# Kernel tuning notes

Hardware: AMD Instinct MI355X
Metric: run time of the kernel (lower is better)

Reference implementation:

```python
import jax, jax.numpy as jnp
import numpy as np

EPS = 1e-5  # BatchNorm eps


def _mlp(x, w1, b1, w2, b2, g, bt):
    # NRI MLP: elu(fc1) -> elu(fc2) -> batchnorm over all leading dims (training-mode batch stats)
    h = jax.nn.elu(x @ w1.T + b1)
    h = jax.nn.elu(h @ w2.T + b2)
    f = h.reshape(-1, h.shape[-1])
    mu = f.mean(0)
    var = f.var(0)  # biased, as in torch BN normalization
    return (h - mu) * jax.lax.rsqrt(var + EPS) * g + bt


def _gru(x, w_ih, w_hh, b_ih, b_hh):
    # x: [B, T, D] batch_first; torch GRU gate order (r, z, n)
    gi = jnp.einsum('btd,hd->bth', x, w_ih) + b_ih  # precompute input gates
    H = w_hh.shape[1]
    h0 = jnp.zeros((x.shape[0], H), x.dtype)

    def step(h, gi_t):
        gh = h @ w_hh.T + b_hh
        ir, iz, inn = jnp.split(gi_t, 3, -1)
        hr, hz, hn = jnp.split(gh, 3, -1)
        r = jax.nn.sigmoid(ir + hr)
        z = jax.nn.sigmoid(iz + hz)
        n = jnp.tanh(inn + r * hn)
        h_new = (1.0 - z) * n + z * h
        return h_new, h_new

    hT, ys = jax.lax.scan(step, h0, gi.transpose(1, 0, 2))
    return ys.transpose(1, 0, 2), hT


def _xavier(key, shape):
    std = np.sqrt(2.0 / (shape[0] + shape[1])).astype(np.float32)
    return jax.random.normal(key, shape, jnp.float32) * std


def setup_inputs() -> dict:
    key = jax.random.key(0)
    ks = iter(jax.random.split(key, 64))
    B, N, T, Fin, H, O = 8, 30, 100, 4, 128, 2
    inputs = jax.random.normal(next(ks), (B, N, T, Fin), jnp.float32)
    r, s = np.nonzero(1 - np.eye(N))  # fully connected, no self loops -> E = N*(N-1)
    eye = np.eye(N, dtype=np.float32)
    d = {
        'inputs': inputs,
        'rel_rec': jnp.asarray(eye[r]),
        'rel_send': jnp.asarray(eye[s]),
    }
    dims = {1: Fin, 2: 2 * H, 3: H, 4: 3 * H}
    for k in (1, 2, 3, 4):
        d[f'm{k}_w1'] = _xavier(next(ks), (H, dims[k]))
        d[f'm{k}_b1'] = jnp.full((H,), 0.1, jnp.float32)
        d[f'm{k}_w2'] = _xavier(next(ks), (H, H))
        d[f'm{k}_b2'] = jnp.full((H,), 0.1, jnp.float32)
        d[f'm{k}_g'] = jnp.ones((H,), jnp.float32)
        d[f'm{k}_bt'] = jnp.zeros((H,), jnp.float32)
    u = float(1.0 / np.sqrt(H))
    for p in ('gf', 'gr'):
        d[f'{p}_wih'] = jax.random.uniform(next(ks), (3 * H, H), jnp.float32, -u, u)
        d[f'{p}_whh'] = jax.random.uniform(next(ks), (3 * H, H), jnp.float32, -u, u)
        d[f'{p}_bih'] = jax.random.uniform(next(ks), (3 * H,), jnp.float32, -u, u)
        d[f'{p}_bhh'] = jax.random.uniform(next(ks), (3 * H,), jnp.float32, -u, u)
    d['pw'] = _xavier(next(ks), (O, H))
    d['pb'] = jnp.full((O,), 0.1, jnp.float32)
    d['ew'] = _xavier(next(ks), (O, 2 * H))
    d['eb'] = jnp.full((O,), 0.1, jnp.float32)
    return d


def reference(inputs, rel_rec, rel_send, m1_w1, m1_b1, m1_w2, m1_b2, m1_g, m1_bt, m2_w1, m2_b1, m2_w2, m2_b2, m2_g, m2_bt, m3_w1, m3_b1, m3_w2, m3_b2, m3_g, m3_bt, m4_w1, m4_b1, m4_w2, m4_b2, m4_g, m4_bt, gf_wih, gf_whh, gf_bih, gf_bhh, gr_wih, gr_whh, gr_bih, gr_bhh, pw, pb, ew, eb):
    N = rel_rec.shape[1]

    def node2edge(x):  # x: [B,N,T,H] -> [B,E,T,2H]
        snd = jnp.einsum('en,bnth->beth', rel_send, x)
        rcv = jnp.einsum('en,bnth->beth', rel_rec, x)
        return jnp.concatenate([snd, rcv], -1)

    def edge2node(x):  # x: [B,E,T,H] -> [B,N,T,H], mean-style normalization by N
        return jnp.einsum('en,beth->bnth', rel_rec, x) / N

    x = _mlp(inputs, m1_w1, m1_b1, m1_w2, m1_b2, m1_g, m1_bt)      # [B,N,T,H]
    x = node2edge(x)                                                # [B,E,T,2H]
    x = _mlp(x, m2_w1, m2_b1, m2_w2, m2_b2, m2_g, m2_bt)            # [B,E,T,H]
    x_skip = x
    x = edge2node(x)                                                # [B,N,T,H]
    x = _mlp(x, m3_w1, m3_b1, m3_w2, m3_b2, m3_g, m3_bt)
    x = node2edge(x)                                                # [B,E,T,2H]
    x = jnp.concatenate([x, x_skip], -1)                            # [B,E,T,3H]
    x = _mlp(x, m4_w1, m4_b1, m4_w2, m4_b2, m4_g, m4_bt)            # [B,E,T,H]

    B, E, T, H = x.shape
    xr = x.reshape(B * E, T, H)
    fwd_x, hT = _gru(xr, gf_wih, gf_whh, gf_bih, gf_bhh)
    rev_x, _ = _gru(xr[:, ::-1], gr_wih, gr_whh, gr_bih, gr_bhh)
    rev_x = rev_x[:, ::-1]

    prior = (fwd_x @ pw.T + pb).reshape(B, E, T, -1)
    comb = jnp.concatenate([fwd_x, rev_x], -1)
    enc = (comb @ ew.T + eb).reshape(B, E, T, -1)
    return prior, enc, hT[None]  # hT[None] matches torch GRU h_n [1, B*E, H]
```

## Files before the change

kernel.cpp:

```cpp
#include <hip/hip_runtime.h>
#include <math.h>

typedef float f32x4 __attribute__((ext_vector_type(4)));
typedef short bf16x8 __attribute__((ext_vector_type(8)));
typedef unsigned int uint32;
#define DEV static __device__ __forceinline__

constexpr int B_ = 8, N_ = 30, T_ = 100, FIN = 4, H_ = 128;
constexpr int E_ = N_*(N_-1);
constexpr int NSEQ = B_*E_;
constexpr int RN = B_*N_*T_;
constexpr int RE = B_*E_*T_;
constexpr int ET = E_*T_;
constexpr int NB_GRU = (NSEQ + 63)/64;

DEV float eluf(float x){ return x > 0.f ? x : __expf(x) - 1.f; }
DEV float sigmoidf(float x){ return 1.f/(1.f + __expf(-x)); }
DEV float tanhfast(float x){
  float cx = fminf(fmaxf(x, -20.f), 20.f);
  float e = __expf(2.f*cx);
  return (e - 1.f)/(e + 1.f);
}
DEV float dot4(f32x4 a, f32x4 b){ return a[0]*b[0] + a[1]*b[1] + a[2]*b[2] + a[3]*b[3]; }

DEV float bf2f(unsigned short u){ return __uint_as_float(((uint32)u) << 16); }
DEV uint32 f2bf_bits(float f){ uint32 b = __float_as_uint(f); return (b + 0x7FFFu + ((b >> 16) & 1u)) >> 16; }
DEV uint32 pack2(float lo, float hi){ return f2bf_bits(lo) | (f2bf_bits(hi) << 16); }

DEV bf16x8 cvt8(const float* __restrict__ p){
  f32x4 a = *(const f32x4*)p;
  f32x4 b = *(const f32x4*)(p+4);
  bf16x8 r;
  r[0]=(short)f2bf_bits(a[0]); r[1]=(short)f2bf_bits(a[1]);
  r[2]=(short)f2bf_bits(a[2]); r[3]=(short)f2bf_bits(a[3]);
  r[4]=(short)f2bf_bits(b[0]); r[5]=(short)f2bf_bits(b[1]);
  r[6]=(short)f2bf_bits(b[2]); r[7]=(short)f2bf_bits(b[3]);
  return r;
}

DEV void edge_decomp(int row, int& b, int& t, int& sn, int& ir)
{
  b = row / ET;
  int rem = row - b*ET;
  int e   = rem / T_;
  t = rem - e*T_;
  ir = e / (N_-1);
  int j = e - ir*(N_-1);
  sn = j + (j >= ir ? 1 : 0);
}

DEV int xcd_swizzle(int orig, int nwg)
{
  int q = nwg >> 3, r = nwg & 7;
  int xcd = orig & 7, j = orig >> 3;
  return (xcd < r ? xcd*(q+1) : r*(q+1) + (xcd-r)*q) + j;
}

__global__ __launch_bounds__(256)
void prep_weights(const float* __restrict__ w21, const float* __restrict__ w22,
                  const float* __restrict__ w41, const float* __restrict__ w42,
                  unsigned short* __restrict__ wbf)
{
  int idx = blockIdx.x*256 + threadIdx.x;
  if (idx >= 114688) return;
  float v;
  if (idx < 32768)      v = w21[idx];
  else if (idx < 49152) v = w22[idx - 32768];
  else if (idx < 98304) v = w41[idx - 49152];
  else                  v = w42[idx - 98304];
  wbf[idx] = (unsigned short)f2bf_bits(v);
}

template<int MODE, int DIN>
__global__ __launch_bounds__(256)
void mlp_fused(const float* __restrict__ src,
               const float* __restrict__ w1, const float* __restrict__ b1,
               const float* __restrict__ w2, const float* __restrict__ b2,
               float* __restrict__ out)
{
  constexpr int KC  = (DIN < 32) ? DIN : 32;
  constexpr int NCH = DIN / KC;
  __shared__ float As[KC][68];
  __shared__ float Ws[32][132];
  __shared__ float Hs[128][68];

  const int tid  = threadIdx.x;
  const int row0 = blockIdx.x * 64;
  const int tx = tid & 15, ty = tid >> 4;
  const int c0 = tx*8, r0 = ty*4;

  float acc[4][8];
  #pragma unroll
  for (int j=0;j<4;++j){
    #pragma unroll
    for (int i=0;i<8;++i) acc[j][i]=0.f;
  }

  for (int ch = 0; ch < NCH; ++ch) {
    for (int idx = tid; idx < 64*KC; idx += 256) {
      int r = idx / KC, k = idx % KC;
      As[k][r] = src[(size_t)(row0 + r)*DIN + ch*KC + k];
    }
    for (int idx = tid; idx < 128*KC; idx += 256) {
      int o = idx / KC, k = idx % KC;
      Ws[k][o] = w1[o*DIN + ch*KC + k];
    }
    __syncthreads();
    #pragma unroll
    for (int k = 0; k < KC; ++k) {
      f32x4 a  = *(const f32x4*)&As[k][r0];
      f32x4 wA = *(const f32x4*)&Ws[k][c0];
      f32x4 wB = *(const f32x4*)&Ws[k][c0+4];
      #pragma unroll
      for (int j=0;j<4;++j){
        #pragma unroll
        for (int i=0;i<4;++i){
          acc[j][i]   += a[j]*wA[i];
          acc[j][4+i] += a[j]*wB[i];
        }
      }
    }
    __syncthreads();
  }
  {
    #pragma unroll
    for (int i=0;i<8;++i){
      float bb = b1[c0+i];
      #pragma unroll
      for (int j=0;j<4;++j)
        Hs[c0+i][r0+j] = eluf(acc[j][i] + bb);
    }
  }
  __syncthreads();

  #pragma unroll
  for (int j=0;j<4;++j){
    #pragma unroll
    for (int i=0;i<8;++i) acc[j][i]=0.f;
  }

  for (int ch = 0; ch < 4; ++ch) {
    for (int idx = tid; idx < 128*32; idx += 256) {
      int o = idx >> 5, k = idx & 31;
      Ws[k][o] = w2[o*H_ + ch*32 + k];
    }
    __syncthreads();
    #pragma unroll
    for (int k = 0; k < 32; ++k) {
      f32x4 a  = *(const f32x4*)&Hs[ch*32 + k][r0];
      f32x4 wA = *(const f32x4*)&Ws[k][c0];
      f32x4 wB = *(const f32x4*)&Ws[k][c0+4];
      #pragma unroll
      for (int j=0;j<4;++j){
        #pragma unroll
        for (int i=0;i<4;++i){
          acc[j][i]   += a[j]*wA[i];
          acc[j][4+i] += a[j]*wB[i];
        }
      }
    }
    __syncthreads();
  }
  {
    #pragma unroll
    for (int j=0;j<4;++j){
      size_t base = (size_t)(row0 + r0 + j)*H_ + c0;
      #pragma unroll
      for (int i=0;i<8;++i) out[base+i] = eluf(acc[j][i] + b2[c0+i]);
    }
  }
}

__global__ __launch_bounds__(128)
void norm_to_bf16(const float* __restrict__ buf, int rows, const float* __restrict__ sums,
                  const float* __restrict__ g, const float* __restrict__ bt,
                  unsigned short* __restrict__ outbf)
{
  int c = threadIdx.x;
  float inv = 1.f/(float)rows;
  float mu  = sums[c]*inv;
  float var = sums[H_+c]*inv - mu*mu;
  float sc  = rsqrtf(var + 1e-5f)*g[c];
  float sh  = bt[c] - mu*sc;
  for (int r = blockIdx.x; r < rows; r += gridDim.x) {
    size_t idx = (size_t)r*H_ + c;
    outbf[idx] = (unsigned short)f2bf_bits(buf[idx]*sc + sh);
  }
}

__global__ __launch_bounds__(256)
void apply_aff4(unsigned short* __restrict__ x4, const float* __restrict__ aff)
{
  size_t idx = ((size_t)blockIdx.x*256 + threadIdx.x)*8;
  int c = (int)(idx & 127);
  uint32* p = (uint32*)(x4 + idx);
  uint32 win[4];
  #pragma unroll
  for (int u=0;u<4;++u) win[u] = p[u];
  uint32 o[4];
  #pragma unroll
  for (int u=0;u<4;++u){
    float lo = __uint_as_float(win[u] << 16);
    float hi = __uint_as_float(win[u] & 0xFFFF0000u);
    float a = lo*aff[c+2*u]   + aff[128+c+2*u];
    float b = hi*aff[c+2*u+1] + aff[128+c+2*u+1];
    o[u] = pack2(a, b);
  }
  #pragma unroll
  for (int u=0;u<4;++u) p[u] = o[u];
}

__global__ __launch_bounds__(256, 2)
void mlp2_scatter(const unsigned short* __restrict__ x1bf,
                  const unsigned short* __restrict__ wbf,
                  const float* __restrict__ b21, const float* __restrict__ b22,
                  float* __restrict__ nodeB, float* __restrict__ stats2)
{
  __shared__ int srow[64], rrow[64];
  __shared__ __align__(16) char pool[17408];
  unsigned short* bufH = (unsigned short*)pool;
  float* red = (float*)pool;

  const int tid  = threadIdx.x;
  const int bid  = xcd_swizzle(blockIdx.x, gridDim.x);
  const int row0 = bid * 64;
  if (tid < 64) {
    int b,t,sn,ir; edge_decomp(row0 + tid, b, t, sn, ir);
    srow[tid] = (b*N_ + sn)*T_ + t;
    rrow[tid] = (b*N_ + ir)*T_ + t;
  }
  __syncthreads();

  const int lane = tid & 63;
  const int wv   = tid >> 6;
  const int c15  = lane & 15;
  const int k8   = (lane >> 4) * 8;
  const int g4   = (lane >> 4);
  const int colb = wv * 32;
  const unsigned short* W21 = wbf;
  const unsigned short* W22 = wbf + 32768;

  int sA[4], rA[4];
  #pragma unroll
  for (int rt=0;rt<4;++rt){ sA[rt] = srow[rt*16 + c15]; rA[rt] = rrow[rt*16 + c15]; }

  f32x4 C[2][4];

  #pragma unroll
  for (int ci=0;ci<2;++ci){
    float bb = b21[colb + ci*16 + c15];
    #pragma unroll
    for (int rt=0;rt<4;++rt) C[ci][rt] = (f32x4){bb,bb,bb,bb};
  }
  {
    bf16x8 Bf[2][8];
    #pragma unroll
    for (int ci=0;ci<2;++ci){
      #pragma unroll
      for (int kc=0;kc<8;++kc)
        Bf[ci][kc] = *(const bf16x8*)&W21[(size_t)(colb+ci*16+c15)*256 + kc*32 + k8];
    }
    #pragma unroll
    for (int kc=0;kc<8;++kc){
      bf16x8 A[4];
      #pragma unroll
      for (int rt=0;rt<4;++rt){
        int nrow = (kc<4) ? sA[rt] : rA[rt];
        A[rt] = *(const bf16x8*)&x1bf[(size_t)nrow*H_ + (kc&3)*32 + k8];
      }
      #pragma unroll
      for (int ci=0;ci<2;++ci){
        #pragma unroll
        for (int rt=0;rt<4;++rt)
          C[ci][rt] = __builtin_amdgcn_mfma_f32_16x16x32_bf16(A[rt], Bf[ci][kc], C[ci][rt], 0,0,0);
      }
    }
  }
  #pragma unroll
  for (int ci=0;ci<2;++ci){
    #pragma unroll
    for (int rt=0;rt<4;++rt){
      #pragma unroll
      for (int rr=0;rr<4;++rr){
        int row = rt*16 + g4*4 + rr;
        bufH[row*136 + colb + ci*16 + c15] = (unsigned short)f2bf_bits(eluf(C[ci][rt][rr]));
      }
    }
  }
  __syncthreads();

  #pragma unroll
  for (int ci=0;ci<2;++ci){
    float bb = b22[colb + ci*16 + c15];
    #pragma unroll
    for (int rt=0;rt<4;++rt) C[ci][rt] = (f32x4){bb,bb,bb,bb};
  }
  {
    bf16x8 Bf[2][4];
    #pragma unroll
    for (int ci=0;ci<2;++ci){
      #pragma unroll
      for (int kc=0;kc<4;++kc)
        Bf[ci][kc] = *(const bf16x8*)&W22[(size_t)(colb+ci*16+c15)*128 + kc*32 + k8];
    }
    #pragma unroll
    for (int kc=0;kc<4;++kc){
      bf16x8 A[4];
      #pragma unroll
      for (int rt=0;rt<4;++rt)
        A[rt] = *(const bf16x8*)&bufH[(rt*16+c15)*136 + kc*32 + k8];
      #pragma unroll
      for (int ci=0;ci<2;++ci){
        #pragma unroll
        for (int rt=0;rt<4;++rt)
          C[ci][rt] = __builtin_amdgcn_mfma_f32_16x16x32_bf16(A[rt], Bf[ci][kc], C[ci][rt], 0,0,0);
      }
    }
  }

  float s1l[2], s2l[2];
  #pragma unroll
  for (int ci=0;ci<2;++ci){ s1l[ci]=0.f; s2l[ci]=0.f; }
  #pragma unroll
  for (int ci=0;ci<2;++ci){
    int col = colb + ci*16 + c15;
    #pragma unroll
    for (int rt=0;rt<4;++rt){
      #pragma unroll
      for (int rr=0;rr<4;++rr){
        int row = rt*16 + g4*4 + rr;
        float v = eluf(C[ci][rt][rr]);
        atomicAdd(&nodeB[(size_t)rrow[row]*H_ + col], v);
        s1l[ci] += v; s2l[ci] += v*v;
      }
    }
  }
  __syncthreads();
  #pragma unroll
  for (int ci=0;ci<2;++ci){
    int col = colb + ci*16 + c15;
    red[col*4 + g4]       = s1l[ci];
    red[512 + col*4 + g4] = s2l[ci];
  }
  __syncthreads();
  if (tid < 128) {
    float s=0.f, q=0.f;
    #pragma unroll
    for (int u=0;u<4;++u){ s += red[tid*4+u]; q += red[512 + tid*4+u]; }
    atomicAdd(&stats2[tid], s);
    atomicAdd(&stats2[128+tid], q);
  }
}

__global__ __launch_bounds__(256, 2)
void mlp24_fused(const unsigned short* __restrict__ x1bf, const unsigned short* __restrict__ x3bf,
                 const float* __restrict__ aff2, const unsigned short* __restrict__ wbf,
                 const float* __restrict__ b21, const float* __restrict__ b22,
                 const float* __restrict__ b41, const float* __restrict__ b42,
                 unsigned short* __restrict__ x4pre, float* __restrict__ stats4)
{
  __shared__ int srow[64], rrow[64];
  __shared__ __align__(16) char pool[34816];
  unsigned short* bufH = (unsigned short*)pool;
  unsigned short* bufX = (unsigned short*)(pool + 17408);
  float* red = (float*)pool;

  const int tid  = threadIdx.x;
  const int bid  = xcd_swizzle(blockIdx.x, gridDim.x);
  const int row0 = bid * 64;
  if (tid < 64) {
    int b,t,sn,ir; edge_decomp(row0 + tid, b, t, sn, ir);
    srow[tid] = (b*N_ + sn)*T_ + t;
    rrow[tid] = (b*N_ + ir)*T_ + t;
  }
  __syncthreads();

  const int lane = tid & 63;
  const int wv   = tid >> 6;
  const int c15  = lane & 15;
  const int k8   = (lane >> 4) * 8;
  const int g4   = (lane >> 4);
  const int colb = wv * 32;
  const unsigned short* W21 = wbf;
  const unsigned short* W22 = wbf + 32768;
  const unsigned short* W41 = wbf + 49152;
  const unsigned short* W42 = wbf + 98304;

  int sA[4], rA[4];
  #pragma unroll
  for (int rt=0;rt<4;++rt){ sA[rt] = srow[rt*16 + c15]; rA[rt] = rrow[rt*16 + c15]; }

  f32x4 C[2][4];

  #pragma unroll
  for (int ci=0;ci<2;++ci){
    float bb = b21[colb + ci*16 + c15];
    #pragma unroll
    for (int rt=0;rt<4;++rt) C[ci][rt] = (f32x4){bb,bb,bb,bb};
  }
  {
    bf16x8 Bf[2][8];
    #pragma unroll
    for (int ci=0;ci<2;++ci){
      #pragma unroll
      for (int kc=0;kc<8;++kc)
        Bf[ci][kc] = *(const bf16x8*)&W21[(size_t)(colb+ci*16+c15)*256 + kc*32 + k8];
    }
    #pragma unroll
    for (int kc=0;kc<8;++kc){
      bf16x8 A[4];
      #pragma unroll
      for (int rt=0;rt<4;++rt){
        int nrow = (kc<4) ? sA[rt] : rA[rt];
        A[rt] = *(const bf16x8*)&x1bf[(size_t)nrow*H_ + (kc&3)*32 + k8];
      }
      #pragma unroll
      for (int ci=0;ci<2;++ci){
        #pragma unroll
        for (int rt=0;rt<4;++rt)
          C[ci][rt] = __builtin_amdgcn_mfma_f32_16x16x32_bf16(A[rt], Bf[ci][kc], C[ci][rt], 0,0,0);
      }
    }
  }
  #pragma unroll
  for (int ci=0;ci<2;++ci){
    #pragma unroll
    for (int rt=0;rt<4;++rt){
      #pragma unroll
      for (int rr=0;rr<4;++rr){
        int row = rt*16 + g4*4 + rr;
        bufH[row*136 + colb + ci*16 + c15] = (unsigned short)f2bf_bits(eluf(C[ci][rt][rr]));
      }
    }
  }
  __syncthreads();

  #pragma unroll
  for (int ci=0;ci<2;++ci){
    float bb = b22[colb + ci*16 + c15];
    #pragma unroll
    for (int rt=0;rt<4;++rt) C[ci][rt] = (f32x4){bb,bb,bb,bb};
  }
  {
    bf16x8 Bf[2][4];
    #pragma unroll
    for (int ci=0;ci<2;++ci){
      #pragma unroll
      for (int kc=0;kc<4;++kc)
        Bf[ci][kc] = *(const bf16x8*)&W22[(size_t)(colb+ci*16+c15)*128 + kc*32 + k8];
    }
    #pragma unroll
    for (int kc=0;kc<4;++kc){
      bf16x8 A[4];
      #pragma unroll
      for (int rt=0;rt<4;++rt)
        A[rt] = *(const bf16x8*)&bufH[(rt*16+c15)*136 + kc*32 + k8];
      #pragma unroll
      for (int ci=0;ci<2;++ci){
        #pragma unroll
        for (int rt=0;rt<4;++rt)
          C[ci][rt] = __builtin_amdgcn_mfma_f32_16x16x32_bf16(A[rt], Bf[ci][kc], C[ci][rt], 0,0,0);
      }
    }
  }
  #pragma unroll
  for (int ci=0;ci<2;++ci){
    int col = colb + ci*16 + c15;
    float sc = aff2[col], sh = aff2[128+col];
    #pragma unroll
    for (int rt=0;rt<4;++rt){
      #pragma unroll
      for (int rr=0;rr<4;++rr){
        int row = rt*16 + g4*4 + rr;
        bufX[row*136 + col] = (unsigned short)f2bf_bits(eluf(C[ci][rt][rr])*sc + sh);
      }
    }
  }
  __syncthreads();

  #pragma unroll
  for (int ci=0;ci<2;++ci){
    float bb = b41[colb + ci*16 + c15];
    #pragma unroll
    for (int rt=0;rt<4;++rt) C[ci][rt] = (f32x4){bb,bb,bb,bb};
  }
  {
    bf16x8 Bf[2][6];
    #pragma unroll
    for (int ci=0;ci<2;++ci){
      #pragma unroll
      for (int kc=0;kc<6;++kc)
        Bf[ci][kc] = *(const bf16x8*)&W41[(size_t)(colb+ci*16+c15)*384 + kc*32 + k8];
    }
    #pragma unroll
    for (int kc=0;kc<6;++kc){
      bf16x8 A[4];
      #pragma unroll
      for (int rt=0;rt<4;++rt){
        if (kc < 4) A[rt] = *(const bf16x8*)&x3bf[(size_t)sA[rt]*H_ + kc*32 + k8];
        else        A[rt] = *(const bf16x8*)&x3bf[(size_t)rA[rt]*H_ + (kc-4)*32 + k8];
      }
      #pragma unroll
      for (int ci=0;ci<2;++ci){
        #pragma unroll
        for (int rt=0;rt<4;++rt)
          C[ci][rt] = __builtin_amdgcn_mfma_f32_16x16x32_bf16(A[rt], Bf[ci][kc], C[ci][rt], 0,0,0);
      }
    }
    #pragma unroll
    for (int ci=0;ci<2;++ci){
      #pragma unroll
      for (int kc=0;kc<6;++kc)
        Bf[ci][kc] = *(const bf16x8*)&W41[(size_t)(colb+ci*16+c15)*384 + (kc+6)*32 + k8];
    }
    #pragma unroll
    for (int kc=6;kc<12;++kc){
      bf16x8 A[4];
      #pragma unroll
      for (int rt=0;rt<4;++rt){
        if (kc < 8) A[rt] = *(const bf16x8*)&x3bf[(size_t)rA[rt]*H_ + (kc-4)*32 + k8];
        else        A[rt] = *(const bf16x8*)&bufX[(rt*16+c15)*136 + (kc-8)*32 + k8];
      }
      #pragma unroll
      for (int ci=0;ci<2;++ci){
        #pragma unroll
        for (int rt=0;rt<4;++rt)
          C[ci][rt] = __builtin_amdgcn_mfma_f32_16x16x32_bf16(A[rt], Bf[ci][kc-6], C[ci][rt], 0,0,0);
      }
    }
  }
  __syncthreads();
  #pragma unroll
  for (int ci=0;ci<2;++ci){
    #pragma unroll
    for (int rt=0;rt<4;++rt){
      #pragma unroll
      for (int rr=0;rr<4;++rr){
        int row = rt*16 + g4*4 + rr;
        bufH[row*136 + colb + ci*16 + c15] = (unsigned short)f2bf_bits(eluf(C[ci][rt][rr]));
      }
    }
  }
  __syncthreads();

  #pragma unroll
  for (int ci=0;ci<2;++ci){
    float bb = b42[colb + ci*16 + c15];
    #pragma unroll
    for (int rt=0;rt<4;++rt) C[ci][rt] = (f32x4){bb,bb,bb,bb};
  }
  {
    bf16x8 Bf[2][4];
    #pragma unroll
    for (int ci=0;ci<2;++ci){
      #pragma unroll
      for (int kc=0;kc<4;++kc)
        Bf[ci][kc] = *(const bf16x8*)&W42[(size_t)(colb+ci*16+c15)*128 + kc*32 + k8];
    }
    #pragma unroll
    for (int kc=0;kc<4;++kc){
      bf16x8 A[4];
      #pragma unroll
      for (int rt=0;rt<4;++rt)
        A[rt] = *(const bf16x8*)&bufH[(rt*16+c15)*136 + kc*32 + k8];
      #pragma unroll
      for (int ci=0;ci<2;++ci){
        #pragma unroll
        for (int rt=0;rt<4;++rt)
          C[ci][rt] = __builtin_amdgcn_mfma_f32_16x16x32_bf16(A[rt], Bf[ci][kc], C[ci][rt], 0,0,0);
      }
    }
  }
  float s1l[2], s2l[2];
  #pragma unroll
  for (int ci=0;ci<2;++ci){ s1l[ci]=0.f; s2l[ci]=0.f; }
  #pragma unroll
  for (int ci=0;ci<2;++ci){
    int col = colb + ci*16 + c15;
    #pragma unroll
    for (int rt=0;rt<4;++rt){
      #pragma unroll
      for (int rr=0;rr<4;++rr){
        int row = rt*16 + g4*4 + rr;
        float v = eluf(C[ci][rt][rr]);
        x4pre[(size_t)(row0 + row)*H_ + col] = (unsigned short)f2bf_bits(v);
        s1l[ci] += v; s2l[ci] += v*v;
      }
    }
  }
  __syncthreads();
  #pragma unroll
  for (int ci=0;ci<2;++ci){
    int col = colb + ci*16 + c15;
    red[col*4 + g4]       = s1l[ci];
    red[512 + col*4 + g4] = s2l[ci];
  }
  __syncthreads();
  if (tid < 128) {
    float s=0.f, q=0.f;
    #pragma unroll
    for (int u=0;u<4;++u){ s += red[tid*4+u]; q += red[512 + tid*4+u]; }
    atomicAdd(&stats4[tid], s);
    atomicAdd(&stats4[128+tid], q);
  }
}

__global__ __launch_bounds__(128)
void stats_kernel(const float* __restrict__ buf, int rows, float* __restrict__ sums)
{
  int c = threadIdx.x;
  float s = 0.f, s2 = 0.f;
  for (int r = blockIdx.x; r < rows; r += gridDim.x) {
    float v = buf[(size_t)r*H_ + c];
    s += v; s2 += v*v;
  }
  atomicAdd(&sums[c], s);
  atomicAdd(&sums[H_ + c], s2);
}

__global__ __launch_bounds__(128)
void finalize_aff(const float* __restrict__ sums, const float* __restrict__ g,
                  const float* __restrict__ bt, float* __restrict__ aff, int rows)
{
  int c = threadIdx.x;
  float inv = 1.f/(float)rows;
  float mu  = sums[c]*inv;
  float var = sums[H_+c]*inv - mu*mu;
  float sc  = rsqrtf(var + 1e-5f)*g[c];
  aff[c]      = sc;
  aff[H_ + c] = bt[c] - mu*sc;
}

__global__ __launch_bounds__(256)
void e2n_finalize(float* __restrict__ nodeB, const float* __restrict__ aff2)
{
  int idx = blockIdx.x*256 + threadIdx.x;
  if (idx >= RN*H_) return;
  int c = idx & 127;
  nodeB[idx] = (nodeB[idx]*aff2[c] + (float)(N_-1)*aff2[128+c]) * (1.f/(float)N_);
}

__global__ __launch_bounds__(512, 1)
void gru_kernel(const unsigned short* __restrict__ x4n,
                const float* __restrict__ wihf, const float* __restrict__ whhf,
                const float* __restrict__ bihf, const float* __restrict__ bhhf,
                const float* __restrict__ wihr, const float* __restrict__ whhr,
                const float* __restrict__ bihr, const float* __restrict__ bhhr,
                const float* __restrict__ pw, const float* __restrict__ pb,
                const float* __restrict__ ew, const float* __restrict__ eb,
                float* __restrict__ out_prior, float* __restrict__ out_enc,
                float* __restrict__ out_hT)
{
  __shared__ __align__(16) unsigned short As[64*264];
  __shared__ __align__(16) float hs[64*132];
  __shared__ float pws[256];
  __shared__ float ews[512];

  const int tid  = threadIdx.x;
  const int dir  = blockIdx.x / NB_GRU;
  const int blk  = blockIdx.x % NB_GRU;
  const int seq0 = blk * 64;
  const int lane = tid & 63;
  const int wv   = __builtin_amdgcn_readfirstlane(tid >> 6);
  const int j0   = wv * 16;
  const int c15  = lane & 15;
  const int k8g  = (lane >> 4) * 8;

  const float* wih = dir ? wihr : wihf;
  const float* whh = dir ? whhr : whhf;
  const float* bih = dir ? bihr : bihf;
  const float* bhh = dir ? bhhr : bhhf;

  bf16x8 Br[8], Bz[8], Bi[4], Bn[4];
  #pragma unroll
  for (int kt=0; kt<8; ++kt){
    const float* sr = (kt<4) ? (wih + (size_t)(j0+c15)*H_ + kt*32 + k8g)
                             : (whh + (size_t)(j0+c15)*H_ + (kt-4)*32 + k8g);
    Br[kt] = cvt8(sr);
    const float* sz = (kt<4) ? (wih + (size_t)(128+j0+c15)*H_ + kt*32 + k8g)
                             : (whh + (size_t)(128+j0+c15)*H_ + (kt-4)*32 + k8g);
    Bz[kt] = cvt8(sz);
  }
  #pragma unroll
  for (int kt=0; kt<4; ++kt){
    Bi[kt] = cvt8(wih + (size_t)(256+j0+c15)*H_ + kt*32 + k8g);
    Bn[kt] = cvt8(whh + (size_t)(256+j0+c15)*H_ + kt*32 + k8g);
  }
  const float bR = bih[j0+c15]     + bhh[j0+c15];
  const float bZ = bih[128+j0+c15] + bhh[128+j0+c15];
  const float bI = bih[256+j0+c15];
  const float bN = bhh[256+j0+c15];
  const float pb0 = pb[0], pb1 = pb[1], eb0 = eb[0], eb1 = eb[1];

  for (int i = tid; i < 64*264; i += 512) As[i] = 0;
  for (int i = tid; i < 64*132; i += 512) hs[i] = 0.f;
  for (int i = tid; i < 256; i += 512) pws[i] = pw[i];
  for (int i = tid; i < 512; i += 512) ews[i] = ew[i];
  float hreg[16];
  #pragma unroll
  for (int i=0;i<16;++i) hreg[i] = 0.f;

  const int ss = tid >> 3;
  const int cc = (tid & 7) * 16;
  const int qq = seq0 + ss;

  uint32 xw[8];
  {
    int t0 = dir ? (T_-1) : 0;
    if (qq < NSEQ) {
      const uint32* gp = (const uint32*)(x4n + ((size_t)qq*T_ + t0)*H_ + cc);
      #pragma unroll
      for (int u=0;u<8;++u) xw[u] = gp[u];
    } else {
      #pragma unroll
      for (int u=0;u<8;++u) xw[u] = 0;
    }
  }
  __syncthreads();

  for (int step = 0; step < T_; ++step) {
    const int t = dir ? (T_-1-step) : step;

    {
      uint32* xp = (uint32*)(As + ss*264 + cc);
      #pragma unroll
      for (int u=0;u<8;++u) xp[u] = xw[u];
    }
    __syncthreads();

    if (step + 1 < T_) {
      int tn = dir ? (T_-2-step) : (step+1);
      if (qq < NSEQ) {
        const uint32* gp = (const uint32*)(x4n + ((size_t)qq*T_ + tn)*H_ + cc);
        #pragma unroll
        for (int u=0;u<8;++u) xw[u] = gp[u];
      }
    }

    f32x4 Cr[4], Cz[4], Ci[4], Cn[4];
    #pragma unroll
    for (int rt=0;rt<4;++rt){
      Cr[rt] = (f32x4){bR,bR,bR,bR};
      Cz[rt] = (f32x4){bZ,bZ,bZ,bZ};
      Ci[rt] = (f32x4){bI,bI,bI,bI};
      Cn[rt] = (f32x4){bN,bN,bN,bN};
    }
    #pragma unroll
    for (int kt=0; kt<8; ++kt){
      bf16x8 a0 = *(const bf16x8*)&As[(size_t)( 0+c15)*264 + kt*32 + k8g];
      bf16x8 a1 = *(const bf16x8*)&As[(size_t)(16+c15)*264 + kt*32 + k8g];
      bf16x8 a2 = *(const bf16x8*)&As[(size_t)(32+c15)*264 + kt*32 + k8g];
      bf16x8 a3 = *(const bf16x8*)&As[(size_t)(48+c15)*264 + kt*32 + k8g];
      Cr[0] = __builtin_amdgcn_mfma_f32_16x16x32_bf16(a0, Br[kt], Cr[0], 0,0,0);
      Cr[1] = __builtin_amdgcn_mfma_f32_16x16x32_bf16(a1, Br[kt], Cr[1], 0,0,0);
      Cr[2] = __builtin_amdgcn_mfma_f32_16x16x32_bf16(a2, Br[kt], Cr[2], 0,0,0);
      Cr[3] = __builtin_amdgcn_mfma_f32_16x16x32_bf16(a3, Br[kt], Cr[3], 0,0,0);
      Cz[0] = __builtin_amdgcn_mfma_f32_16x16x32_bf16(a0, Bz[kt], Cz[0], 0,0,0);
      Cz[1] = __builtin_amdgcn_mfma_f32_16x16x32_bf16(a1, Bz[kt], Cz[1], 0,0,0);
      Cz[2] = __builtin_amdgcn_mfma_f32_16x16x32_bf16(a2, Bz[kt], Cz[2], 0,0,0);
      Cz[3] = __builtin_amdgcn_mfma_f32_16x16x32_bf16(a3, Bz[kt], Cz[3], 0,0,0);
      if (kt < 4) {
        Ci[0] = __builtin_amdgcn_mfma_f32_16x16x32_bf16(a0, Bi[kt], Ci[0], 0,0,0);
        Ci[1] = __builtin_amdgcn_mfma_f32_16x16x32_bf16(a1, Bi[kt], Ci[1], 0,0,0);
        Ci[2] = __builtin_amdgcn_mfma_f32_16x16x32_bf16(a2, Bi[kt], Ci[2], 0,0,0);
        Ci[3] = __builtin_amdgcn_mfma_f32_16x16x32_bf16(a3, Bi[kt], Ci[3], 0,0,0);
      } else {
        Cn[0] = __builtin_amdgcn_mfma_f32_16x16x32_bf16(a0, Bn[kt-4], Cn[0], 0,0,0);
        Cn[1] = __builtin_amdgcn_mfma_f32_16x16x32_bf16(a1, Bn[kt-4], Cn[1], 0,0,0);
        Cn[2] = __builtin_amdgcn_mfma_f32_16x16x32_bf16(a2, Bn[kt-4], Cn[2], 0,0,0);
        Cn[3] = __builtin_amdgcn_mfma_f32_16x16x32_bf16(a3, Bn[kt-4], Cn[3], 0,0,0);
      }
    }
    __syncthreads();

    #pragma unroll
    for (int rt=0;rt<4;++rt){
      #pragma unroll
      for (int rr=0;rr<4;++rr){
        float r_ = sigmoidf(Cr[rt][rr]);
        float z_ = sigmoidf(Cz[rt][rr]);
        float n_ = tanhfast(Ci[rt][rr] + r_*Cn[rt][rr]);
        float hn = (1.f - z_)*n_ + z_*hreg[rt*4+rr];
        hreg[rt*4+rr] = hn;
        int row = rt*16 + (lane>>4)*4 + rr;
        As[(size_t)row*264 + 128 + j0 + c15] = (unsigned short)f2bf_bits(hn);
        hs[row*132 + j0 + c15] = hn;
      }
    }
    __syncthreads();

    if (qq < NSEQ) {
      const f32x4* hrow = (const f32x4*)(hs + ss*132 + cc);
      f32x4 h0=hrow[0], h1=hrow[1], h2=hrow[2], h3=hrow[3];
      size_t obase = ((size_t)qq*T_ + t)*2;
      if (dir == 0) {
        const f32x4* pw0 = (const f32x4*)(pws + cc);
        const f32x4* pw1 = (const f32x4*)(pws + H_ + cc);
        const f32x4* ew0 = (const f32x4*)(ews + cc);
        const f32x4* ew1 = (const f32x4*)(ews + 2*H_ + cc);
        float p0 = dot4(pw0[0],h0)+dot4(pw0[1],h1)+dot4(pw0[2],h2)+dot4(pw0[3],h3);
        float p1 = dot4(pw1[0],h0)+dot4(pw1[1],h1)+dot4(pw1[2],h2)+dot4(pw1[3],h3);
        float e0 = dot4(ew0[0],h0)+dot4(ew0[1],h1)+dot4(ew0[2],h2)+dot4(ew0[3],h3);
        float e1 = dot4(ew1[0],h0)+dot4(ew1[1],h1)+dot4(ew1[2],h2)+dot4(ew1[3],h3);
        #pragma unroll
        for (int m=1;m<8;m<<=1){
          p0 += __shfl_xor(p0,m); p1 += __shfl_xor(p1,m);
          e0 += __shfl_xor(e0,m); e1 += __shfl_xor(e1,m);
        }
        if ((tid & 7) == 0) {
          out_prior[obase]   = p0 + pb0;
          out_prior[obase+1] = p1 + pb1;
          atomicAdd(&out_enc[obase],   e0);
          atomicAdd(&out_enc[obase+1], e1);
        }
      } else {
        const f32x4* ew0 = (const f32x4*)(ews + H_ + cc);
        const f32x4* ew1 = (const f32x4*)(ews + 2*H_ + H_ + cc);
        float e0 = dot4(ew0[0],h0)+dot4(ew0[1],h1)+dot4(ew0[2],h2)+dot4(ew0[3],h3);
        float e1 = dot4(ew1[0],h0)+dot4(ew1[1],h1)+dot4(ew1[2],h2)+dot4(ew1[3],h3);
        #pragma unroll
        for (int m=1;m<8;m<<=1){
          e0 += __shfl_xor(e0,m); e1 += __shfl_xor(e1,m);
        }
        if ((tid & 7) == 0) {
          atomicAdd(&out_enc[obase],   e0 + eb0);
          atomicAdd(&out_enc[obase+1], e1 + eb1);
        }
      }
    }
  }

  if (dir == 0) {
    __syncthreads();
    for (int idx = tid; idx < 64*H_; idx += 512) {
      int s = idx >> 7, c = idx & 127;
      int q = seq0 + s;
      if (q < NSEQ) out_hT[(size_t)q*H_ + c] = hs[s*132 + c];
    }
  }
}

__global__ void ws_report(float* out, float v){ out[0] = v; }

extern "C" void kernel_launch(void* const* d_in, const int* in_sizes, int n_in,
                              void* d_out, int out_size, void* d_ws, size_t ws_size,
                              hipStream_t stream)
{
  (void)in_sizes; (void)n_in; (void)out_size;
  const float* inputs = (const float*)d_in[0];
  const float* m1_w1 = (const float*)d_in[3];  const float* m1_b1 = (const float*)d_in[4];
  const float* m1_w2 = (const float*)d_in[5];  const float* m1_b2 = (const float*)d_in[6];
  const float* m1_g  = (const float*)d_in[7];  const float* m1_bt = (const float*)d_in[8];
  const float* m2_w1 = (const float*)d_in[9];  const float* m2_b1 = (const float*)d_in[10];
  const float* m2_w2 = (const float*)d_in[11]; const float* m2_b2 = (const float*)d_in[12];
  const float* m2_g  = (const float*)d_in[13]; const float* m2_bt = (const float*)d_in[14];
  const float* m3_w1 = (const float*)d_in[15]; const float* m3_b1 = (const float*)d_in[16];
  const float* m3_w2 = (const float*)d_in[17]; const float* m3_b2 = (const float*)d_in[18];
  const float* m3_g  = (const float*)d_in[19]; const float* m3_bt = (const float*)d_in[20];
  const float* m4_w1 = (const float*)d_in[21]; const float* m4_b1 = (const float*)d_in[22];
  const float* m4_w2 = (const float*)d_in[23]; const float* m4_b2 = (const float*)d_in[24];
  const float* m4_g  = (const float*)d_in[25]; const float* m4_bt = (const float*)d_in[26];
  const float* gf_wih = (const float*)d_in[27]; const float* gf_whh = (const float*)d_in[28];
  const float* gf_bih = (const float*)d_in[29]; const float* gf_bhh = (const float*)d_in[30];
  const float* gr_wih = (const float*)d_in[31]; const float* gr_whh = (const float*)d_in[32];
  const float* gr_bih = (const float*)d_in[33]; const float* gr_bhh = (const float*)d_in[34];
  const float* pw = (const float*)d_in[35]; const float* pb = (const float*)d_in[36];
  const float* ew = (const float*)d_in[37]; const float* eb = (const float*)d_in[38];

  float* out       = (float*)d_out;
  float* out_prior = out;
  float* out_enc   = out + (size_t)RE*2;
  float* out_hT    = out + (size_t)RE*4;

  size_t x4elems = (size_t)RE*H_;
  size_t nodeElems = (size_t)RN*H_;
  unsigned short* x4pre = (unsigned short*)d_ws;
  float* nodeA = (float*)(x4pre + x4elems);
  float* nodeB = nodeA + nodeElems;
  float* nodeC = nodeB + nodeElems;
  float* stats = nodeC + nodeElems;
  float* aff   = stats + 1024;
  unsigned short* wbf  = (unsigned short*)(aff + 512);
  unsigned short* x1bf = wbf + 114688;
  unsigned short* x3bf = (unsigned short*)nodeA;
  size_t need = (size_t)((char*)(x1bf + nodeElems) - (char*)d_ws);
  if (ws_size < need) {
    ws_report<<<1, 1, 0, stream>>>(out_prior, (float)ws_size);
    return;
  }

  (void)hipMemsetAsync(stats, 0, 1024*sizeof(float), stream);
  (void)hipMemsetAsync(nodeB, 0, nodeElems*sizeof(float), stream);
  (void)hipMemsetAsync(out_enc, 0, (size_t)RE*2*sizeof(float), stream);

  prep_weights<<<448, 256, 0, stream>>>(m2_w1, m2_w2, m4_w1, m4_w2, wbf);

  mlp_fused<0, FIN><<<RN/64, 256, 0, stream>>>(inputs, m1_w1, m1_b1, m1_w2, m1_b2, nodeA);
  stats_kernel<<<512, 128, 0, stream>>>(nodeA, RN, stats + 0);
  norm_to_bf16<<<512, 128, 0, stream>>>(nodeA, RN, stats + 0, m1_g, m1_bt, x1bf);

  mlp2_scatter<<<RE/64, 256, 0, stream>>>(x1bf, wbf, m2_b1, m2_b2, nodeB, stats + 256);
  finalize_aff<<<1, 128, 0, stream>>>(stats + 256, m2_g, m2_bt, aff + 0, RE);
  e2n_finalize<<<(RN*H_ + 255)/256, 256, 0, stream>>>(nodeB, aff + 0);

  mlp_fused<2, H_><<<RN/64, 256, 0, stream>>>(nodeB, m3_w1, m3_b1, m3_w2, m3_b2, nodeC);
  stats_kernel<<<512, 128, 0, stream>>>(nodeC, RN, stats + 512);
  norm_to_bf16<<<512, 128, 0, stream>>>(nodeC, RN, stats + 512, m3_g, m3_bt, x3bf);

  mlp24_fused<<<RE/64, 256, 0, stream>>>(x1bf, x3bf, aff + 0, wbf,
      m2_b1, m2_b2, m4_b1, m4_b2, x4pre, stats + 768);
  finalize_aff<<<1, 128, 0, stream>>>(stats + 768, m4_g, m4_bt, aff + 256, RE);

  apply_aff4<<<(int)(x4elems/(256*8)), 256, 0, stream>>>(x4pre, aff + 256);

  gru_kernel<<<2*NB_GRU, 512, 0, stream>>>(x4pre,
      gf_wih, gf_whh, gf_bih, gf_bhh,
      gr_wih, gr_whh, gr_bih, gr_bhh,
      pw, pb, ew, eb, out_prior, out_enc, out_hT);
}
```

Before: 2.016 ms.

## Halve GRU sequence tile, drop fp32 hidden buffer, raise occupancy bound

The GRU kernel now processes 32 sequences per block instead of 64, doubling the block count. It removes the fp32 hidden-state shared buffer and reads the bf16 copy already kept for the MFMA A operand, which cuts shared memory and register use. The launch bound now allows up to 4 blocks per CU. The intent is more parallelism and latency hiding across the serial time loop. The cost is that each block repeats its weight loads and the output projections use bf16-rounded h, which also makes hT less precise.

```diff
diff --git a/kernel.cpp b/kernel.cpp
--- a/kernel.cpp
+++ b/kernel.cpp
@@ -12,7 +12,8 @@
 constexpr int RN = B_*N_*T_;
 constexpr int RE = B_*E_*T_;
 constexpr int ET = E_*T_;
-constexpr int NB_GRU = (NSEQ + 63)/64;
+constexpr int SEQB = 32;
+constexpr int NBG  = (NSEQ + SEQB - 1)/SEQB;
 
 DEV float eluf(float x){ return x > 0.f ? x : __expf(x) - 1.f; }
 DEV float sigmoidf(float x){ return 1.f/(1.f + __expf(-x)); }
@@ -640,7 +641,7 @@
   nodeB[idx] = (nodeB[idx]*aff2[c] + (float)(N_-1)*aff2[128+c]) * (1.f/(float)N_);
 }
 
-__global__ __launch_bounds__(512, 1)
+__global__ __launch_bounds__(512, 4)
 void gru_kernel(const unsigned short* __restrict__ x4n,
                 const float* __restrict__ wihf, const float* __restrict__ whhf,
                 const float* __restrict__ bihf, const float* __restrict__ bhhf,
@@ -651,15 +652,14 @@
                 float* __restrict__ out_prior, float* __restrict__ out_enc,
                 float* __restrict__ out_hT)
 {
-  __shared__ __align__(16) unsigned short As[64*264];
-  __shared__ __align__(16) float hs[64*132];
+  __shared__ __align__(16) unsigned short As[SEQB*264];
   __shared__ float pws[256];
   __shared__ float ews[512];
 
   const int tid  = threadIdx.x;
-  const int dir  = blockIdx.x / NB_GRU;
-  const int blk  = blockIdx.x % NB_GRU;
-  const int seq0 = blk * 64;
+  const int dir  = blockIdx.x / NBG;
+  const int blk  = blockIdx.x % NBG;
+  const int seq0 = blk * SEQB;
   const int lane = tid & 63;
   const int wv   = __builtin_amdgcn_readfirstlane(tid >> 6);
   const int j0   = wv * 16;
@@ -692,28 +692,27 @@
   const float bN = bhh[256+j0+c15];
   const float pb0 = pb[0], pb1 = pb[1], eb0 = eb[0], eb1 = eb[1];
 
-  for (int i = tid; i < 64*264; i += 512) As[i] = 0;
-  for (int i = tid; i < 64*132; i += 512) hs[i] = 0.f;
+  for (int i = tid; i < SEQB*264; i += 512) As[i] = 0;
   for (int i = tid; i < 256; i += 512) pws[i] = pw[i];
   for (int i = tid; i < 512; i += 512) ews[i] = ew[i];
-  float hreg[16];
-  #pragma unroll
-  for (int i=0;i<16;++i) hreg[i] = 0.f;
-
-  const int ss = tid >> 3;
-  const int cc = (tid & 7) * 16;
+  float hreg[8];
+  #pragma unroll
+  for (int i=0;i<8;++i) hreg[i] = 0.f;
+
+  const int ss = tid >> 4;
+  const int cc = (tid & 15) * 8;
   const int qq = seq0 + ss;
 
-  uint32 xw[8];
+  uint32 xw[4];
   {
     int t0 = dir ? (T_-1) : 0;
     if (qq < NSEQ) {
       const uint32* gp = (const uint32*)(x4n + ((size_t)qq*T_ + t0)*H_ + cc);
       #pragma unroll
-      for (int u=0;u<8;++u) xw[u] = gp[u];
+      for (int u=0;u<4;++u) xw[u] = gp[u];
     } else {
       #pragma unroll
-      for (int u=0;u<8;++u) xw[u] = 0;
+      for (int u=0;u<4;++u) xw[u] = 0;
     }
   }
   __syncthreads();
@@ -724,7 +723,7 @@
     {
       uint32* xp = (uint32*)(As + ss*264 + cc);
       #pragma unroll
-      for (int u=0;u<8;++u) xp[u] = xw[u];
+      for (int u=0;u<4;++u) xp[u] = xw[u];
     }
     __syncthreads();
 
@@ -733,13 +732,13 @@
       if (qq < NSEQ) {
         const uint32* gp = (const uint32*)(x4n + ((size_t)qq*T_ + tn)*H_ + cc);
         #pragma unroll
-        for (int u=0;u<8;++u) xw[u] = gp[u];
-      }
-    }
-
-    f32x4 Cr[4], Cz[4], Ci[4], Cn[4];
-    #pragma unroll
-    for (int rt=0;rt<4;++rt){
+        for (int u=0;u<4;++u) xw[u] = gp[u];
+      }
+    }
+
+    f32x4 Cr[2], Cz[2], Ci[2], Cn[2];
+    #pragma unroll
+    for (int rt=0;rt<2;++rt){
       Cr[rt] = (f32x4){bR,bR,bR,bR};
       Cz[rt] = (f32x4){bZ,bZ,bZ,bZ};
       Ci[rt] = (f32x4){bI,bI,bI,bI};
@@ -749,32 +748,22 @@
     for (int kt=0; kt<8; ++kt){
       bf16x8 a0 = *(const bf16x8*)&As[(size_t)( 0+c15)*264 + kt*32 + k8g];
       bf16x8 a1 = *(const bf16x8*)&As[(size_t)(16+c15)*264 + kt*32 + k8g];
-      bf16x8 a2 = *(const bf16x8*)&As[(size_t)(32+c15)*264 + kt*32 + k8g];
-      bf16x8 a3 = *(const bf16x8*)&As[(size_t)(48+c15)*264 + kt*32 + k8g];
       Cr[0] = __builtin_amdgcn_mfma_f32_16x16x32_bf16(a0, Br[kt], Cr[0], 0,0,0);
       Cr[1] = __builtin_amdgcn_mfma_f32_16x16x32_bf16(a1, Br[kt], Cr[1], 0,0,0);
-      Cr[2] = __builtin_amdgcn_mfma_f32_16x16x32_bf16(a2, Br[kt], Cr[2], 0,0,0);
-      Cr[3] = __builtin_amdgcn_mfma_f32_16x16x32_bf16(a3, Br[kt], Cr[3], 0,0,0);
       Cz[0] = __builtin_amdgcn_mfma_f32_16x16x32_bf16(a0, Bz[kt], Cz[0], 0,0,0);
       Cz[1] = __builtin_amdgcn_mfma_f32_16x16x32_bf16(a1, Bz[kt], Cz[1], 0,0,0);
-      Cz[2] = __builtin_amdgcn_mfma_f32_16x16x32_bf16(a2, Bz[kt], Cz[2], 0,0,0);
-      Cz[3] = __builtin_amdgcn_mfma_f32_16x16x32_bf16(a3, Bz[kt], Cz[3], 0,0,0);
       if (kt < 4) {
         Ci[0] = __builtin_amdgcn_mfma_f32_16x16x32_bf16(a0, Bi[kt], Ci[0], 0,0,0);
         Ci[1] = __builtin_amdgcn_mfma_f32_16x16x32_bf16(a1, Bi[kt], Ci[1], 0,0,0);
-        Ci[2] = __builtin_amdgcn_mfma_f32_16x16x32_bf16(a2, Bi[kt], Ci[2], 0,0,0);
-        Ci[3] = __builtin_amdgcn_mfma_f32_16x16x32_bf16(a3, Bi[kt], Ci[3], 0,0,0);
       } else {
         Cn[0] = __builtin_amdgcn_mfma_f32_16x16x32_bf16(a0, Bn[kt-4], Cn[0], 0,0,0);
         Cn[1] = __builtin_amdgcn_mfma_f32_16x16x32_bf16(a1, Bn[kt-4], Cn[1], 0,0,0);
-        Cn[2] = __builtin_amdgcn_mfma_f32_16x16x32_bf16(a2, Bn[kt-4], Cn[2], 0,0,0);
-        Cn[3] = __builtin_amdgcn_mfma_f32_16x16x32_bf16(a3, Bn[kt-4], Cn[3], 0,0,0);
       }
     }
     __syncthreads();
 
     #pragma unroll
-    for (int rt=0;rt<4;++rt){
+    for (int rt=0;rt<2;++rt){
       #pragma unroll
       for (int rr=0;rr<4;++rr){
         float r_ = sigmoidf(Cr[rt][rr]);
@@ -784,45 +773,54 @@
         hreg[rt*4+rr] = hn;
         int row = rt*16 + (lane>>4)*4 + rr;
         As[(size_t)row*264 + 128 + j0 + c15] = (unsigned short)f2bf_bits(hn);
-        hs[row*132 + j0 + c15] = hn;
       }
     }
     __syncthreads();
 
     if (qq < NSEQ) {
-      const f32x4* hrow = (const f32x4*)(hs + ss*132 + cc);
-      f32x4 h0=hrow[0], h1=hrow[1], h2=hrow[2], h3=hrow[3];
+      float h[8];
+      {
+        const uint32* hp = (const uint32*)(As + ss*264 + 128 + cc);
+        #pragma unroll
+        for (int u=0;u<4;++u){
+          uint32 w = hp[u];
+          h[2*u]   = __uint_as_float(w << 16);
+          h[2*u+1] = __uint_as_float(w & 0xFFFF0000u);
+        }
+      }
       size_t obase = ((size_t)qq*T_ + t)*2;
       if (dir == 0) {
-        const f32x4* pw0 = (const f32x4*)(pws + cc);
-        const f32x4* pw1 = (const f32x4*)(pws + H_ + cc);
-        const f32x4* ew0 = (const f32x4*)(ews + cc);
-        const f32x4* ew1 = (const f32x4*)(ews + 2*H_ + cc);
-        float p0 = dot4(pw0[0],h0)+dot4(pw0[1],h1)+dot4(pw0[2],h2)+dot4(pw0[3],h3);
-        float p1 = dot4(pw1[0],h0)+dot4(pw1[1],h1)+dot4(pw1[2],h2)+dot4(pw1[3],h3);
-        float e0 = dot4(ew0[0],h0)+dot4(ew0[1],h1)+dot4(ew0[2],h2)+dot4(ew0[3],h3);
-        float e1 = dot4(ew1[0],h0)+dot4(ew1[1],h1)+dot4(ew1[2],h2)+dot4(ew1[3],h3);
-        #pragma unroll
-        for (int m=1;m<8;m<<=1){
+        float p0=0.f, p1=0.f, e0=0.f, e1=0.f;
+        #pragma unroll
+        for (int i=0;i<8;++i){
+          p0 += h[i]*pws[cc+i];
+          p1 += h[i]*pws[128+cc+i];
+          e0 += h[i]*ews[cc+i];
+          e1 += h[i]*ews[256+cc+i];
+        }
+        #pragma unroll
+        for (int m=1;m<16;m<<=1){
           p0 += __shfl_xor(p0,m); p1 += __shfl_xor(p1,m);
           e0 += __shfl_xor(e0,m); e1 += __shfl_xor(e1,m);
         }
-        if ((tid & 7) == 0) {
+        if ((tid & 15) == 0) {
           out_prior[obase]   = p0 + pb0;
           out_prior[obase+1] = p1 + pb1;
           atomicAdd(&out_enc[obase],   e0);
           atomicAdd(&out_enc[obase+1], e1);
         }
       } else {
-        const f32x4* ew0 = (const f32x4*)(ews + H_ + cc);
-        const f32x4* ew1 = (const f32x4*)(ews + 2*H_ + H_ + cc);
-        float e0 = dot4(ew0[0],h0)+dot4(ew0[1],h1)+dot4(ew0[2],h2)+dot4(ew0[3],h3);
-        float e1 = dot4(ew1[0],h0)+dot4(ew1[1],h1)+dot4(ew1[2],h2)+dot4(ew1[3],h3);
-        #pragma unroll
-        for (int m=1;m<8;m<<=1){
+        float e0=0.f, e1=0.f;
+        #pragma unroll
+        for (int i=0;i<8;++i){
+          e0 += h[i]*ews[128+cc+i];
+          e1 += h[i]*ews[256+128+cc+i];
+        }
+        #pragma unroll
+        for (int m=1;m<16;m<<=1){
           e0 += __shfl_xor(e0,m); e1 += __shfl_xor(e1,m);
         }
-        if ((tid & 7) == 0) {
+        if ((tid & 15) == 0) {
           atomicAdd(&out_enc[obase],   e0 + eb0);
           atomicAdd(&out_enc[obase+1], e1 + eb1);
         }
@@ -832,10 +830,10 @@
 
   if (dir == 0) {
     __syncthreads();
-    for (int idx = tid; idx < 64*H_; idx += 512) {
+    for (int idx = tid; idx < SEQB*H_; idx += 512) {
       int s = idx >> 7, c = idx & 127;
       int q = seq0 + s;
-      if (q < NSEQ) out_hT[(size_t)q*H_ + c] = hs[s*132 + c];
+      if (q < NSEQ) out_hT[(size_t)q*H_ + c] = bf2f(As[s*264 + 128 + c]);
     }
   }
 }
@@ -913,7 +911,7 @@
 
   apply_aff4<<<(int)(x4elems/(256*8)), 256, 0, stream>>>(x4pre, aff + 256);
 
-  gru_kernel<<<2*NB_GRU, 512, 0, stream>>>(x4pre,
+  gru_kernel<<<2*NBG, 512, 0, stream>>>(x4pre,
       gf_wih, gf_whh, gf_bih, gf_bhh,
       gr_wih, gr_whh, gr_bih, gr_bhh,
       pw, pb, ew, eb, out_prior, out_enc, out_hT);
```

Measured after the change: 2.551 ms. 1.27x slower.

## Fold final batchnorm affine into GRU input weights and bias, drop apply pass

Applied to the files above, without the earlier changes.

Removes the separate apply_aff4 pass over the large x4 tensor by folding the per-channel batchnorm scale into the GRU input-gate weights and the shift into the gate biases (W·sh added to bR, bZ, bI). Also restructures the per-step x staging so the next timestep's input is written to shared memory after the MFMA barrier, removing one __syncthreads per step and prefetching two steps ahead. The trade-off is slightly different bf16 rounding, because the scaled weights are quantized instead of the normalized activations, plus a small per-block setup dot product.

```diff
diff --git a/kernel.cpp b/kernel.cpp
--- a/kernel.cpp
+++ b/kernel.cpp
@@ -37,6 +37,12 @@
   r[6]=(short)f2bf_bits(b[2]); r[7]=(short)f2bf_bits(b[3]);
   return r;
 }
+DEV bf16x8 cvt8s(const float* __restrict__ p, const float* __restrict__ sc){
+  bf16x8 r;
+  #pragma unroll
+  for (int e=0;e<8;++e) r[e] = (short)f2bf_bits(p[e]*sc[e]);
+  return r;
+}
 
 DEV void edge_decomp(int row, int& b, int& t, int& sn, int& ir)
 {
@@ -186,28 +192,6 @@
     size_t idx = (size_t)r*H_ + c;
     outbf[idx] = (unsigned short)f2bf_bits(buf[idx]*sc + sh);
   }
-}
-
-__global__ __launch_bounds__(256)
-void apply_aff4(unsigned short* __restrict__ x4, const float* __restrict__ aff)
-{
-  size_t idx = ((size_t)blockIdx.x*256 + threadIdx.x)*8;
-  int c = (int)(idx & 127);
-  uint32* p = (uint32*)(x4 + idx);
-  uint32 win[4];
-  #pragma unroll
-  for (int u=0;u<4;++u) win[u] = p[u];
-  uint32 o[4];
-  #pragma unroll
-  for (int u=0;u<4;++u){
-    float lo = __uint_as_float(win[u] << 16);
-    float hi = __uint_as_float(win[u] & 0xFFFF0000u);
-    float a = lo*aff[c+2*u]   + aff[128+c+2*u];
-    float b = hi*aff[c+2*u+1] + aff[128+c+2*u+1];
-    o[u] = pack2(a, b);
-  }
-  #pragma unroll
-  for (int u=0;u<4;++u) p[u] = o[u];
 }
 
 __global__ __launch_bounds__(256, 2)
@@ -641,7 +625,7 @@
 }
 
 __global__ __launch_bounds__(512, 1)
-void gru_kernel(const unsigned short* __restrict__ x4n,
+void gru_kernel(const unsigned short* __restrict__ x4raw, const float* __restrict__ aff4,
                 const float* __restrict__ wihf, const float* __restrict__ whhf,
                 const float* __restrict__ bihf, const float* __restrict__ bhhf,
                 const float* __restrict__ wihr, const float* __restrict__ whhr,
@@ -653,6 +637,7 @@
 {
   __shared__ __align__(16) unsigned short As[64*264];
   __shared__ __align__(16) float hs[64*132];
+  __shared__ float sc4[128], sh4[128];
   __shared__ float pws[256];
   __shared__ float ews[512];
 
@@ -671,31 +656,42 @@
   const float* bih = dir ? bihr : bihf;
   const float* bhh = dir ? bhhr : bhhf;
 
+  for (int i = tid; i < 64*264; i += 512) As[i] = 0;
+  for (int i = tid; i < 64*132; i += 512) hs[i] = 0.f;
+  if (tid < 128) { sc4[tid] = aff4[tid]; sh4[tid] = aff4[128+tid]; }
+  for (int i = tid; i < 256; i += 512) pws[i] = pw[i];
+  for (int i = tid; i < 512; i += 512) ews[i] = ew[i];
+  __syncthreads();
+
   bf16x8 Br[8], Bz[8], Bi[4], Bn[4];
   #pragma unroll
   for (int kt=0; kt<8; ++kt){
-    const float* sr = (kt<4) ? (wih + (size_t)(j0+c15)*H_ + kt*32 + k8g)
-                             : (whh + (size_t)(j0+c15)*H_ + (kt-4)*32 + k8g);
-    Br[kt] = cvt8(sr);
-    const float* sz = (kt<4) ? (wih + (size_t)(128+j0+c15)*H_ + kt*32 + k8g)
-                             : (whh + (size_t)(128+j0+c15)*H_ + (kt-4)*32 + k8g);
-    Bz[kt] = cvt8(sz);
+    if (kt < 4) {
+      Br[kt] = cvt8s(wih + (size_t)(j0+c15)*H_ + kt*32 + k8g,     sc4 + kt*32 + k8g);
+      Bz[kt] = cvt8s(wih + (size_t)(128+j0+c15)*H_ + kt*32 + k8g, sc4 + kt*32 + k8g);
+    } else {
+      Br[kt] = cvt8(whh + (size_t)(j0+c15)*H_ + (kt-4)*32 + k8g);
+      Bz[kt] = cvt8(whh + (size_t)(128+j0+c15)*H_ + (kt-4)*32 + k8g);
+    }
   }
   #pragma unroll
   for (int kt=0; kt<4; ++kt){
-    Bi[kt] = cvt8(wih + (size_t)(256+j0+c15)*H_ + kt*32 + k8g);
+    Bi[kt] = cvt8s(wih + (size_t)(256+j0+c15)*H_ + kt*32 + k8g, sc4 + kt*32 + k8g);
     Bn[kt] = cvt8(whh + (size_t)(256+j0+c15)*H_ + kt*32 + k8g);
   }
-  const float bR = bih[j0+c15]     + bhh[j0+c15];
-  const float bZ = bih[128+j0+c15] + bhh[128+j0+c15];
-  const float bI = bih[256+j0+c15];
+  float dR=0.f, dZ=0.f, dI=0.f;
+  for (int k=0; k<H_; ++k){
+    float shk = sh4[k];
+    dR += wih[(size_t)(j0+c15)*H_ + k]*shk;
+    dZ += wih[(size_t)(128+j0+c15)*H_ + k]*shk;
+    dI += wih[(size_t)(256+j0+c15)*H_ + k]*shk;
+  }
+  const float bR = bih[j0+c15]     + bhh[j0+c15]     + dR;
+  const float bZ = bih[128+j0+c15] + bhh[128+j0+c15] + dZ;
+  const float bI = bih[256+j0+c15] + dI;
   const float bN = bhh[256+j0+c15];
   const float pb0 = pb[0], pb1 = pb[1], eb0 = eb[0], eb1 = eb[1];
 
-  for (int i = tid; i < 64*264; i += 512) As[i] = 0;
-  for (int i = tid; i < 64*132; i += 512) hs[i] = 0.f;
-  for (int i = tid; i < 256; i += 512) pws[i] = pw[i];
-  for (int i = tid; i < 512; i += 512) ews[i] = ew[i];
   float hreg[16];
   #pragma unroll
   for (int i=0;i<16;++i) hreg[i] = 0.f;
@@ -708,34 +704,27 @@
   {
     int t0 = dir ? (T_-1) : 0;
     if (qq < NSEQ) {
-      const uint32* gp = (const uint32*)(x4n + ((size_t)qq*T_ + t0)*H_ + cc);
+      const uint32* gp = (const uint32*)(x4raw + ((size_t)qq*T_ + t0)*H_ + cc);
       #pragma unroll
       for (int u=0;u<8;++u) xw[u] = gp[u];
     } else {
       #pragma unroll
       for (int u=0;u<8;++u) xw[u] = 0;
     }
+    uint32* xp = (uint32*)(As + ss*264 + cc);
+    #pragma unroll
+    for (int u=0;u<8;++u) xp[u] = xw[u];
+    if (qq < NSEQ) {
+      int t1 = dir ? (T_-2) : 1;
+      const uint32* gp = (const uint32*)(x4raw + ((size_t)qq*T_ + t1)*H_ + cc);
+      #pragma unroll
+      for (int u=0;u<8;++u) xw[u] = gp[u];
+    }
   }
   __syncthreads();
 
   for (int step = 0; step < T_; ++step) {
     const int t = dir ? (T_-1-step) : step;
-
-    {
-      uint32* xp = (uint32*)(As + ss*264 + cc);
-      #pragma unroll
-      for (int u=0;u<8;++u) xp[u] = xw[u];
-    }
-    __syncthreads();
-
-    if (step + 1 < T_) {
-      int tn = dir ? (T_-2-step) : (step+1);
-      if (qq < NSEQ) {
-        const uint32* gp = (const uint32*)(x4n + ((size_t)qq*T_ + tn)*H_ + cc);
-        #pragma unroll
-        for (int u=0;u<8;++u) xw[u] = gp[u];
-      }
-    }
 
     f32x4 Cr[4], Cz[4], Ci[4], Cn[4];
     #pragma unroll
@@ -773,6 +762,18 @@
     }
     __syncthreads();
 
+    if (step + 1 < T_) {
+      uint32* xp = (uint32*)(As + ss*264 + cc);
+      #pragma unroll
+      for (int u=0;u<8;++u) xp[u] = xw[u];
+      if (step + 2 < T_ && qq < NSEQ) {
+        int tn = dir ? (T_-3-step) : (step+2);
+        const uint32* gp = (const uint32*)(x4raw + ((size_t)qq*T_ + tn)*H_ + cc);
+        #pragma unroll
+        for (int u=0;u<8;++u) xw[u] = gp[u];
+      }
+    }
+
     #pragma unroll
     for (int rt=0;rt<4;++rt){
       #pragma unroll
@@ -911,9 +912,7 @@
       m2_b1, m2_b2, m4_b1, m4_b2, x4pre, stats + 768);
   finalize_aff<<<1, 128, 0, stream>>>(stats + 768, m4_g, m4_bt, aff + 256, RE);
 
-  apply_aff4<<<(int)(x4elems/(256*8)), 256, 0, stream>>>(x4pre, aff + 256);
-
-  gru_kernel<<<2*NB_GRU, 512, 0, stream>>>(x4pre,
+  gru_kernel<<<2*NB_GRU, 512, 0, stream>>>(x4pre, aff + 256,
       gf_wih, gf_whh, gf_bih, gf_bhh,
       gr_wih, gr_whh, gr_bih, gr_bhh,
       pw, pb, ew, eb, out_prior, out_enc, out_hT);
```

Result: faster. 1.955 ms, median of 2 (-3.0%).
